# Performance work log

Measured on AMD Instinct MI355X. Metric: run time of the kernel, lower is better.

The kernel has to match this reference:

```python
import jax, jax.numpy as jnp
import numpy as np

D_MODEL = 1024
N_HEADS = 16
D_HEAD = D_MODEL // N_HEADS
BATCH = 2
SEQ = 2048


def setup_inputs() -> dict:
    key = jax.random.key(0)
    ks = jax.random.split(key, 16)
    s = 0.02
    d = D_MODEL
    return {
        "x": jax.random.normal(ks[0], (BATCH, SEQ, d), jnp.float32),
        "Wq": jax.random.normal(ks[1], (d, d), jnp.float32) * s,
        "bq": jnp.zeros((d,), jnp.float32),
        "Wk": jax.random.normal(ks[2], (d, d), jnp.float32) * s,
        "bk": jnp.zeros((d,), jnp.float32),
        "Wv": jax.random.normal(ks[3], (d, d), jnp.float32) * s,
        "bv": jnp.zeros((d,), jnp.float32),
        "Wo": jax.random.normal(ks[4], (d, d), jnp.float32) * s,
        "bo": jnp.zeros((d,), jnp.float32),
        "Wt": jax.random.normal(ks[5], (d, 1), jnp.float32) * s,
        "bt": jnp.zeros((1,), jnp.float32),
        "Wg": jax.random.normal(ks[6], (d, d), jnp.float32) * s,
        "bg": jnp.zeros((d,), jnp.float32),
    }


def _evolved_attention(x, Wq, bq, Wk, bk, Wv, bv, Wo, bo, Wt, bt, Wg, bg):
    B, S, D = x.shape
    H, dh = N_HEADS, D_HEAD

    def heads(y):  # [B,S,D] -> [B,H,S,dh]
        return y.reshape(B, S, H, dh).transpose(0, 2, 1, 3)

    q = heads(x @ Wq + bq)
    k = heads(x @ Wk + bk)
    v = heads(x @ Wv + bv)

    # cosine similarity (F.normalize with eps=1e-12)
    qn = q / jnp.maximum(jnp.linalg.norm(q, axis=-1, keepdims=True), 1e-12)
    kn = k / jnp.maximum(jnp.linalg.norm(k, axis=-1, keepdims=True), 1e-12)
    scores = jnp.einsum("bhqd,bhkd->bhqk", qn, kn)

    # adaptive temperature: sigmoid(temp_proj(mean_s x)) + 0.5, shape [B,1]
    temp = jax.nn.sigmoid(x.mean(axis=1) @ Wt + bt) + 0.5  # [B,1]
    scores = scores / temp[:, None, None, :]  # broadcast [B,1,1,1]

    # sparsemax-style: softmax over top-k (k = S//4), scattered back
    kk = max(1, S // 4)
    vals, idx = jax.lax.top_k(scores, kk)          # [B,H,S,kk]
    w = jax.nn.softmax(vals, axis=-1)
    rows = jnp.arange(B * H * S)[:, None]
    attn = (
        jnp.zeros((B * H * S, S), scores.dtype)
        .at[rows, idx.reshape(-1, kk)]
        .set(w.reshape(-1, kk))
        .reshape(B, H, S, S)
    )

    out = jnp.einsum("bhqk,bhkd->bhqd", attn, v)
    out = out.transpose(0, 2, 1, 3).reshape(B, S, D)
    out = out @ Wo + bo

    # highway gating
    gate = jax.nn.sigmoid(x @ Wg + bg)
    return gate * out + (1.0 - gate) * x


def reference(x, Wq, bq, Wk, bk, Wv, bv, Wo, bo, Wt, bt, Wg, bg):
    return _evolved_attention(x, Wq, bq, Wk, bk, Wv, bv, Wo, bo, Wt, bt, Wg, bg)
```

## Files before the change

kernel.cpp:

```cpp
#include <hip/hip_runtime.h>

typedef unsigned short u16;
typedef __attribute__((ext_vector_type(4))) float f32x4;
typedef __attribute__((ext_vector_type(8))) short bf16x8;
typedef __attribute__((ext_vector_type(4))) int i32x4;

#define BB 2
#define SS 2048
#define DD 1024
#define HH 16
#define DH 64
#define KK 512

#define OFF_SCAL  ((size_t)0)
#define OFF_WT    ((size_t)256)
#define OFF_XB    (OFF_WT + (size_t)5*1024*1024*2)
#define OFF_AO    OFF_XB
#define OFF_QH    (OFF_XB + (size_t)4096*1024*2)
#define OFF_QN    (OFF_QH + (size_t)4096*4096*2)
#define OFF_KN    (OFF_QN + (size_t)4096*1024*2)
#define OFF_VT    (OFF_KN + (size_t)4096*1024*2)

__device__ __forceinline__ float b2f(u16 u) { return __uint_as_float(((unsigned)u) << 16); }
__device__ __forceinline__ u16 f2b(float f) {
    unsigned u = __float_as_uint(f);
    return (u16)((u + 0x7fffu + ((u >> 16) & 1u)) >> 16);
}

__global__ __launch_bounds__(256) void convert_x(const float* x, u16* xb) {
    int i = (blockIdx.x * 256 + threadIdx.x) * 4;
    float4 v = *(const float4*)(x + i);
    u16 r0 = f2b(v.x), r1 = f2b(v.y), r2 = f2b(v.z), r3 = f2b(v.w);
    xb[i] = r0; xb[i + 1] = r1; xb[i + 2] = r2; xb[i + 3] = r3;
}

__global__ __launch_bounds__(256) void transpose_w(
        const float* Wq, const float* Wk, const float* Wv, const float* Wg, const float* Wo,
        u16* WT) {
    int z = blockIdx.z;
    const float* src = (z == 0) ? Wq : (z == 1) ? Wk : (z == 2) ? Wv : (z == 3) ? Wg : Wo;
    u16* dst = WT + (size_t)z * 1024 * 1024;
    __shared__ float tile[64][65];
    int n0 = blockIdx.x * 64, k0 = blockIdx.y * 64;
    int rbase = threadIdx.x >> 6, c = threadIdx.x & 63;
#pragma unroll
    for (int i = 0; i < 16; i++) {
        int r = i * 4 + rbase;
        tile[r][c] = src[(size_t)(k0 + r) * 1024 + n0 + c];
    }
    __syncthreads();
#pragma unroll
    for (int i = 0; i < 16; i++) {
        int r = i * 4 + rbase;
        dst[(size_t)(n0 + r) * 1024 + k0 + c] = f2b(tile[c][r]);
    }
}

__global__ __launch_bounds__(256) void temp_partial(const float* x, const float* Wt,
                                                    float* accbuf) {
    int b = blockIdx.x >> 5, ch = blockIdx.x & 31;
    float a = 0.f;
    for (int si = 0; si < 64; si++) {
        int s = ch * 64 + si;
        const float* xr = x + ((size_t)(b * SS + s)) * DD;
#pragma unroll
        for (int k = 0; k < 4; k++) {
            int c = threadIdx.x + k * 256;
            a += xr[c] * Wt[c];
        }
    }
    for (int o = 32; o; o >>= 1) a += __shfl_xor(a, o);
    __shared__ float red[4];
    if ((threadIdx.x & 63) == 0) red[threadIdx.x >> 6] = a;
    __syncthreads();
    if (threadIdx.x == 0) atomicAdd(&accbuf[b], red[0] + red[1] + red[2] + red[3]);
}

__global__ void temp_final(const float* accbuf, const float* bt, float* itemp) {
    int t = threadIdx.x;
    if (t < BB) {
        float v = accbuf[t] / (float)SS + bt[0];
        float tmp = 1.f / (1.f + __expf(-v)) + 0.5f;
        itemp[t] = 1.f / tmp;
    }
}

__global__ __launch_bounds__(256) void gemm_qkvg(
        const u16* X, const u16* WT,
        const float* bq, const float* bk, const float* bv, const float* bg, u16* Qh) {
    __shared__ u16 la[64 * 40];
    __shared__ u16 lb[64 * 40];
    int tid = threadIdx.x, wid = tid >> 6, lane = tid & 63;
    int m0 = blockIdx.x * 64, n0 = blockIdx.y * 64;
    int quad = lane >> 4, ml = lane & 15;
    f32x4 acc[4];
#pragma unroll
    for (int i = 0; i < 4; i++) acc[i] = (f32x4){0.f, 0.f, 0.f, 0.f};

    int sr = tid >> 2, sg = tid & 3;
    for (int k0 = 0; k0 < 1024; k0 += 32) {
        __syncthreads();
        *(i32x4*)&la[sr * 40 + sg * 8] = *(const i32x4*)&X[(size_t)(m0 + sr) * 1024 + k0 + sg * 8];
        *(i32x4*)&lb[sr * 40 + sg * 8] = *(const i32x4*)&WT[(size_t)(n0 + sr) * 1024 + k0 + sg * 8];
        __syncthreads();
        bf16x8 a = *(const bf16x8*)&la[(wid * 16 + ml) * 40 + quad * 8];
#pragma unroll
        for (int nt = 0; nt < 4; nt++) {
            bf16x8 bfr = *(const bf16x8*)&lb[(nt * 16 + ml) * 40 + quad * 8];
            acc[nt] = __builtin_amdgcn_mfma_f32_16x16x32_bf16(a, bfr, acc[nt], 0, 0, 0);
        }
    }
#pragma unroll
    for (int nt = 0; nt < 4; nt++) {
        int col = n0 + nt * 16 + ml;
        int mat = col >> 10, bc = col & 1023;
        const float* bp = (mat == 0) ? bq : (mat == 1) ? bk : (mat == 2) ? bv : bg;
        float bias = bp[bc];
#pragma unroll
        for (int r = 0; r < 4; r++) {
            int row = m0 + wid * 16 + quad * 4 + r;
            Qh[(size_t)row * 4096 + col] = f2b(acc[nt][r] + bias);
        }
    }
}

__global__ __launch_bounds__(256) void norm_repack(const u16* Qh, u16* qn, u16* kn, u16* vt) {
    int wid = threadIdx.x >> 6, lane = threadIdx.x & 63;
    int idx = blockIdx.x * 4 + wid;
    int token = idx >> 4, h = idx & 15;
    int b = token >> 11, s = token & 2047;
    int bh = b * HH + h;
    const u16* rowp = Qh + (size_t)token * 4096 + h * 64;
    float q = b2f(rowp[lane]);
    float k = b2f(rowp[1024 + lane]);
    u16 v = rowp[2048 + lane];
    float sq = q * q, sk = k * k;
    for (int o = 32; o; o >>= 1) { sq += __shfl_xor(sq, o); sk += __shfl_xor(sk, o); }
    float qd = fmaxf(sqrtf(sq), 1e-12f), kd = fmaxf(sqrtf(sk), 1e-12f);
    qn[((size_t)bh * SS + s) * DH + lane] = f2b(q / qd);
    kn[((size_t)bh * SS + s) * DH + lane] = f2b(k / kd);
    vt[((size_t)bh * DH + lane) * SS + s] = v;
}

#define EST 2088

__global__ __launch_bounds__(1024, 8) void attn_kernel(
        const u16* qn, const u16* kn, const u16* vt, const float* itemp, u16* ao) {
    __shared__ __align__(16) u16 e16[16 * EST];
    __shared__ float pvp[3][16][66];
    __shared__ float zrow_s[16];

    int tid = threadIdx.x, wid = tid >> 6, lane = tid & 63;
    int quad = lane >> 4, nl = lane & 15;
    int bh = blockIdx.x >> 7, qt = blockIdx.x & 127;
    int b = bh >> 4, h = bh & 15;
    const u16* qbase = qn + ((size_t)bh * SS + qt * 16) * DH;
    const u16* kbase = kn + (size_t)bh * SS * DH;
    const u16* vbase = vt + (size_t)bh * DH * SS;
    float it = itemp[b];

    bf16x8 aq0 = *(const bf16x8*)(qbase + nl * DH + quad * 8);
    bf16x8 aq1 = *(const bf16x8*)(qbase + nl * DH + 32 + quad * 8);

#pragma unroll 4
    for (int c = 0; c < 8; c++) {
        int j = c * 256 + wid * 16 + nl;
        const u16* kr = kbase + (size_t)j * DH;
        bf16x8 b0 = *(const bf16x8*)(kr + quad * 8);
        bf16x8 b1 = *(const bf16x8*)(kr + 32 + quad * 8);
        f32x4 acc = (f32x4){0.f, 0.f, 0.f, 0.f};
        acc = __builtin_amdgcn_mfma_f32_16x16x32_bf16(aq0, b0, acc, 0, 0, 0);
        acc = __builtin_amdgcn_mfma_f32_16x16x32_bf16(aq1, b1, acc, 0, 0, 0);
#pragma unroll
        for (int r = 0; r < 4; r++) e16[(quad * 4 + r) * EST + j] = f2b(acc[r] * it);
    }
    __syncthreads();

    {
        int row = wid;
        int key[32];
#pragma unroll
        for (int c = 0; c < 32; c++) {
            int raw = (int)e16[row * EST + c * 64 + lane];
            key[c] = (raw & 0x8000) ? (raw ^ 0xFFFF) : (raw | 0x8000);
        }
        int P = 0;
        for (int bit = 15; bit >= 0; bit--) {
            int cand = P | (1 << bit);
            int cnt = 0;
#pragma unroll
            for (int c = 0; c < 32; c++)
                cnt += (int)__popcll(__ballot(key[c] >= cand));
            if (cnt >= KK) P = cand;
        }
        float z = 0.f;
#pragma unroll
        for (int c = 0; c < 32; c++) {
            float e = 0.f;
            if (key[c] >= P) {
                int raw = (key[c] & 0x8000) ? (key[c] ^ 0x8000) : (key[c] ^ 0xFFFF);
                e = __expf(b2f((u16)raw));
            }
            z += e;
            e16[row * EST + c * 64 + lane] = f2b(e);
        }
#pragma unroll
        for (int o = 32; o; o >>= 1) z += __shfl_xor(z, o);
        if (lane == 0) zrow_s[row] = z;
    }
    __syncthreads();

    f32x4 accp = (f32x4){0.f, 0.f, 0.f, 0.f};
    int kq = wid >> 2, g = wid & 3;
    int dh = g * 16 + nl;
    const u16* vrow = vbase + (size_t)dh * SS;
#pragma unroll 4
    for (int c = 0; c < 8; c++) {
        int j0 = kq * 512 + c * 64;
#pragma unroll
        for (int ks = 0; ks < 2; ks++) {
            bf16x8 a = *(const bf16x8*)&e16[nl * EST + j0 + ks * 32 + quad * 8];
            bf16x8 bfr = *(const bf16x8*)(vrow + j0 + ks * 32 + quad * 8);
            accp = __builtin_amdgcn_mfma_f32_16x16x32_bf16(a, bfr, accp, 0, 0, 0);
        }
    }
    if (kq) {
#pragma unroll
        for (int r = 0; r < 4; r++) pvp[kq - 1][quad * 4 + r][dh] = accp[r];
    }
    __syncthreads();
    if (kq == 0) {
#pragma unroll
        for (int r = 0; r < 4; r++) {
            int q = quad * 4 + r;
            float val = (accp[r] + pvp[0][q][dh] + pvp[1][q][dh] + pvp[2][q][dh]) / zrow_s[q];
            size_t row = (size_t)(b * SS + qt * 16 + q);
            ao[row * DD + h * 64 + dh] = f2b(val);
        }
    }
}

__global__ __launch_bounds__(256) void gemm_out(
        const u16* AO, const u16* WTo, const float* bo,
        const u16* Qh, const float* x, float* out) {
    __shared__ u16 la[64 * 40];
    __shared__ u16 lb[64 * 40];
    int tid = threadIdx.x, wid = tid >> 6, lane = tid & 63;
    int m0 = blockIdx.x * 64, n0 = blockIdx.y * 64;
    int quad = lane >> 4, ml = lane & 15;
    f32x4 acc[4];
#pragma unroll
    for (int i = 0; i < 4; i++) acc[i] = (f32x4){0.f, 0.f, 0.f, 0.f};

    int sr = tid >> 2, sg = tid & 3;
    for (int k0 = 0; k0 < 1024; k0 += 32) {
        __syncthreads();
        *(i32x4*)&la[sr * 40 + sg * 8] = *(const i32x4*)&AO[(size_t)(m0 + sr) * 1024 + k0 + sg * 8];
        *(i32x4*)&lb[sr * 40 + sg * 8] = *(const i32x4*)&WTo[(size_t)(n0 + sr) * 1024 + k0 + sg * 8];
        __syncthreads();
        bf16x8 a = *(const bf16x8*)&la[(wid * 16 + ml) * 40 + quad * 8];
#pragma unroll
        for (int nt = 0; nt < 4; nt++) {
            bf16x8 bfr = *(const bf16x8*)&lb[(nt * 16 + ml) * 40 + quad * 8];
            acc[nt] = __builtin_amdgcn_mfma_f32_16x16x32_bf16(a, bfr, acc[nt], 0, 0, 0);
        }
    }
#pragma unroll
    for (int nt = 0; nt < 4; nt++) {
        int col = n0 + nt * 16 + ml;
        float bias = bo[col];
#pragma unroll
        for (int r = 0; r < 4; r++) {
            int row = m0 + wid * 16 + quad * 4 + r;
            float g = b2f(Qh[(size_t)row * 4096 + 3072 + col]);
            float gate = 1.f / (1.f + __expf(-g));
            float xv = x[(size_t)row * 1024 + col];
            float o = acc[nt][r] + bias;
            out[(size_t)row * 1024 + col] = gate * o + (1.f - gate) * xv;
        }
    }
}

extern "C" void kernel_launch(void* const* d_in, const int* in_sizes, int n_in,
                              void* d_out, int out_size, void* d_ws, size_t ws_size,
                              hipStream_t stream) {
    const float* x  = (const float*)d_in[0];
    const float* Wq = (const float*)d_in[1];
    const float* bq = (const float*)d_in[2];
    const float* Wk = (const float*)d_in[3];
    const float* bk = (const float*)d_in[4];
    const float* Wv = (const float*)d_in[5];
    const float* bv = (const float*)d_in[6];
    const float* Wo = (const float*)d_in[7];
    const float* bo = (const float*)d_in[8];
    const float* Wt = (const float*)d_in[9];
    const float* bt = (const float*)d_in[10];
    const float* Wg = (const float*)d_in[11];
    const float* bg = (const float*)d_in[12];

    char* w = (char*)d_ws;
    float* accbuf = (float*)(w + OFF_SCAL);
    float* itemp  = accbuf + 2;
    u16*   WT     = (u16*)(w + OFF_WT);
    u16*   xb     = (u16*)(w + OFF_XB);
    u16*   ao     = (u16*)(w + OFF_AO);
    u16*   Qh     = (u16*)(w + OFF_QH);
    u16*   qn     = (u16*)(w + OFF_QN);
    u16*   kn     = (u16*)(w + OFF_KN);
    u16*   vt     = (u16*)(w + OFF_VT);

    hipMemsetAsync(accbuf, 0, 2 * sizeof(float), stream);

    convert_x<<<4096, 256, 0, stream>>>(x, xb);
    transpose_w<<<dim3(16, 16, 5), 256, 0, stream>>>(Wq, Wk, Wv, Wg, Wo, WT);
    temp_partial<<<64, 256, 0, stream>>>(x, Wt, accbuf);
    temp_final<<<1, 64, 0, stream>>>(accbuf, bt, itemp);
    gemm_qkvg<<<dim3(64, 64), 256, 0, stream>>>(xb, WT, bq, bk, bv, bg, Qh);
    norm_repack<<<16384, 256, 0, stream>>>(Qh, qn, kn, vt);
    attn_kernel<<<4096, 1024, 0, stream>>>(qn, kn, vt, itemp, ao);
    gemm_out<<<dim3(64, 16), 256, 0, stream>>>(ao, WT + (size_t)4 * 1024 * 1024, bo, Qh, x,
                                               (float*)d_out);
}
```

Baseline: 548.5 us.

## Replace bitwise top-k radix search with two-pass histogram select; tile V transpose

The 16-pass ballot/popcount radix search for the top-k threshold is replaced with a two-level 256-bin histogram built with LDS atomics and packed 16-bit counters, followed by wave-level suffix scans to find the threshold bin and then the low byte. Separately, norm_repack now processes 64 tokens per block and stages V in shared memory so the transposed V store is written as 16-byte coalesced chunks instead of scattered 2-byte stores. The histogram reuses the PV-partial shared buffer as scratch and re-reads scores from LDS rather than holding them in registers. The cost is LDS atomic contention when many keys fall into the same bin.

After: 633.4 us. 1.15x slower.

```diff
diff --git a/kernel.cpp b/kernel.cpp
--- a/kernel.cpp
+++ b/kernel.cpp
@@ -125,21 +125,31 @@
 }
 
 __global__ __launch_bounds__(256) void norm_repack(const u16* Qh, u16* qn, u16* kn, u16* vt) {
-    int wid = threadIdx.x >> 6, lane = threadIdx.x & 63;
-    int idx = blockIdx.x * 4 + wid;
-    int token = idx >> 4, h = idx & 15;
-    int b = token >> 11, s = token & 2047;
-    int bh = b * HH + h;
-    const u16* rowp = Qh + (size_t)token * 4096 + h * 64;
-    float q = b2f(rowp[lane]);
-    float k = b2f(rowp[1024 + lane]);
-    u16 v = rowp[2048 + lane];
-    float sq = q * q, sk = k * k;
-    for (int o = 32; o; o >>= 1) { sq += __shfl_xor(sq, o); sk += __shfl_xor(sk, o); }
-    float qd = fmaxf(sqrtf(sq), 1e-12f), kd = fmaxf(sqrtf(sk), 1e-12f);
-    qn[((size_t)bh * SS + s) * DH + lane] = f2b(q / qd);
-    kn[((size_t)bh * SS + s) * DH + lane] = f2b(k / kd);
-    vt[((size_t)bh * DH + lane) * SS + s] = v;
+    __shared__ u16 vtile[64][72];
+    int tid = threadIdx.x, wid = tid >> 6, lane = tid & 63;
+    int bh = blockIdx.x >> 5, stile = blockIdx.x & 31;
+    int b = bh >> 4, h = bh & 15;
+    int s0 = stile * 64;
+    for (int t = 0; t < 16; t++) {
+        int sl = wid * 16 + t;
+        int s = s0 + sl;
+        const u16* rowp = Qh + ((size_t)(b * SS + s)) * 4096 + h * 64;
+        float q = b2f(rowp[lane]);
+        float k = b2f(rowp[1024 + lane]);
+        u16 v = rowp[2048 + lane];
+        float sq = q * q, sk = k * k;
+        for (int o = 32; o; o >>= 1) { sq += __shfl_xor(sq, o); sk += __shfl_xor(sk, o); }
+        float qd = fmaxf(sqrtf(sq), 1e-12f), kd = fmaxf(sqrtf(sk), 1e-12f);
+        size_t orow = ((size_t)bh * SS + s) * DH;
+        qn[orow + lane] = f2b(q / qd);
+        kn[orow + lane] = f2b(k / kd);
+        vtile[lane][sl] = v;
+    }
+    __syncthreads();
+    int dh = tid >> 2, c0 = (tid & 3) * 16;
+    u16* dst = vt + ((size_t)bh * DH + dh) * SS + s0 + c0;
+    *(i32x4*)dst       = *(const i32x4*)&vtile[dh][c0];
+    *(i32x4*)(dst + 8) = *(const i32x4*)&vtile[dh][c0 + 8];
 }
 
 #define EST 2088
@@ -147,7 +157,7 @@
 __global__ __launch_bounds__(1024, 8) void attn_kernel(
         const u16* qn, const u16* kn, const u16* vt, const float* itemp, u16* ao) {
     __shared__ __align__(16) u16 e16[16 * EST];
-    __shared__ float pvp[3][16][66];
+    __shared__ float shpv[3][16][66];
     __shared__ float zrow_s[16];
 
     int tid = threadIdx.x, wid = tid >> 6, lane = tid & 63;
@@ -178,31 +188,75 @@
 
     {
         int row = wid;
-        int key[32];
-#pragma unroll
+        unsigned* wh = (unsigned*)&shpv[0][0][0] + wid * 132;
+        const u16* rowp = &e16[row * EST];
+        wh[lane] = 0u; wh[64 + lane] = 0u;
+#pragma unroll 4
         for (int c = 0; c < 32; c++) {
-            int raw = (int)e16[row * EST + c * 64 + lane];
-            key[c] = (raw & 0x8000) ? (raw ^ 0xFFFF) : (raw | 0x8000);
-        }
-        int P = 0;
-        for (int bit = 15; bit >= 0; bit--) {
-            int cand = P | (1 << bit);
-            int cnt = 0;
-#pragma unroll
-            for (int c = 0; c < 32; c++)
-                cnt += (int)__popcll(__ballot(key[c] >= cand));
-            if (cnt >= KK) P = cand;
-        }
+            int raw = (int)rowp[c * 64 + lane];
+            int key = (raw & 0x8000) ? (raw ^ 0xFFFF) : (raw | 0x8000);
+            int bin = key >> 8;
+            atomicAdd(&wh[bin >> 1], (bin & 1) ? 65536u : 1u);
+        }
+        unsigned w0 = wh[2 * lane], w1 = wh[2 * lane + 1];
+        unsigned c0 = w0 & 0xFFFFu, c1 = w0 >> 16, c2 = w1 & 0xFFFFu, c3 = w1 >> 16;
+        unsigned suf = c0 + c1 + c2 + c3;
+#pragma unroll
+        for (int o = 1; o < 64; o <<= 1) {
+            unsigned t = __shfl_down(suf, o);
+            suf += (lane + o < 64) ? t : 0u;
+        }
+        unsigned S0 = suf, S1 = suf - c0, S2 = S1 - c1, S3 = S2 - c2;
+        int lb = -1;
+        if (S3 >= (unsigned)KK) lb = 4 * lane + 3;
+        else if (S2 >= (unsigned)KK) lb = 4 * lane + 2;
+        else if (S1 >= (unsigned)KK) lb = 4 * lane + 1;
+        else if (S0 >= (unsigned)KK) lb = 4 * lane;
+#pragma unroll
+        for (int o = 32; o; o >>= 1) { int t = __shfl_xor(lb, o); lb = (t > lb) ? t : lb; }
+        int bstar = lb;
+        int sel = bstar & 3;
+        unsigned cb = (sel == 0) ? c0 : (sel == 1) ? c1 : (sel == 2) ? c2 : c3;
+        unsigned Sb = (sel == 0) ? S0 : (sel == 1) ? S1 : (sel == 2) ? S2 : S3;
+        unsigned nd2 = (unsigned)KK - (Sb - cb);
+        nd2 = (unsigned)__shfl((int)nd2, bstar >> 2);
+        wh[lane] = 0u; wh[64 + lane] = 0u;
+#pragma unroll 4
+        for (int c = 0; c < 32; c++) {
+            int raw = (int)rowp[c * 64 + lane];
+            int key = (raw & 0x8000) ? (raw ^ 0xFFFF) : (raw | 0x8000);
+            if ((key >> 8) == bstar) {
+                int lo = key & 255;
+                atomicAdd(&wh[lo >> 1], (lo & 1) ? 65536u : 1u);
+            }
+        }
+        w0 = wh[2 * lane]; w1 = wh[2 * lane + 1];
+        c0 = w0 & 0xFFFFu; c1 = w0 >> 16; c2 = w1 & 0xFFFFu; c3 = w1 >> 16;
+        suf = c0 + c1 + c2 + c3;
+#pragma unroll
+        for (int o = 1; o < 64; o <<= 1) {
+            unsigned t = __shfl_down(suf, o);
+            suf += (lane + o < 64) ? t : 0u;
+        }
+        S0 = suf; S1 = suf - c0; S2 = S1 - c1; S3 = S2 - c2;
+        lb = -1;
+        if (S3 >= nd2) lb = 4 * lane + 3;
+        else if (S2 >= nd2) lb = 4 * lane + 2;
+        else if (S1 >= nd2) lb = 4 * lane + 1;
+        else if (S0 >= nd2) lb = 4 * lane;
+#pragma unroll
+        for (int o = 32; o; o >>= 1) { int t = __shfl_xor(lb, o); lb = (t > lb) ? t : lb; }
+        int P = (bstar << 8) | lb;
         float z = 0.f;
-#pragma unroll
+        u16* roww = &e16[row * EST];
+#pragma unroll 4
         for (int c = 0; c < 32; c++) {
+            int raw = (int)rowp[c * 64 + lane];
+            int key = (raw & 0x8000) ? (raw ^ 0xFFFF) : (raw | 0x8000);
             float e = 0.f;
-            if (key[c] >= P) {
-                int raw = (key[c] & 0x8000) ? (key[c] ^ 0x8000) : (key[c] ^ 0xFFFF);
-                e = __expf(b2f((u16)raw));
-            }
+            if (key >= P) e = __expf(b2f((u16)raw));
             z += e;
-            e16[row * EST + c * 64 + lane] = f2b(e);
+            roww[c * 64 + lane] = f2b(e);
         }
 #pragma unroll
         for (int o = 32; o; o >>= 1) z += __shfl_xor(z, o);
@@ -226,14 +280,14 @@
     }
     if (kq) {
 #pragma unroll
-        for (int r = 0; r < 4; r++) pvp[kq - 1][quad * 4 + r][dh] = accp[r];
+        for (int r = 0; r < 4; r++) shpv[kq - 1][quad * 4 + r][dh] = accp[r];
     }
     __syncthreads();
     if (kq == 0) {
 #pragma unroll
         for (int r = 0; r < 4; r++) {
             int q = quad * 4 + r;
-            float val = (accp[r] + pvp[0][q][dh] + pvp[1][q][dh] + pvp[2][q][dh]) / zrow_s[q];
+            float val = (accp[r] + shpv[0][q][dh] + shpv[1][q][dh] + shpv[2][q][dh]) / zrow_s[q];
             size_t row = (size_t)(b * SS + qt * 16 + q);
             ao[row * DD + h * 64 + dh] = f2b(val);
         }
@@ -316,7 +370,7 @@
     temp_partial<<<64, 256, 0, stream>>>(x, Wt, accbuf);
     temp_final<<<1, 64, 0, stream>>>(accbuf, bt, itemp);
     gemm_qkvg<<<dim3(64, 64), 256, 0, stream>>>(xb, WT, bq, bk, bv, bg, Qh);
-    norm_repack<<<16384, 256, 0, stream>>>(Qh, qn, kn, vt);
+    norm_repack<<<1024, 256, 0, stream>>>(Qh, qn, kn, vt);
     attn_kernel<<<4096, 1024, 0, stream>>>(qn, kn, vt, itemp, ao);
     gemm_out<<<dim3(64, 16), 256, 0, stream>>>(ao, WT + (size_t)4 * 1024 * 1024, bo, Qh, x,
                                                (float*)d_out);
```
